# Kernel tuning notes

Measured on AMD Instinct MI355X. Metric: run time of the kernel, lower is better.

Reference implementation:

```python
import jax, jax.numpy as jnp
import numpy as np

EPS = 1e-5

def layer_norm(x, g, b):
    mu = jnp.mean(x, axis=-1, keepdims=True)
    var = jnp.mean((x - mu) ** 2, axis=-1, keepdims=True)
    return (x - mu) * jax.lax.rsqrt(var + EPS) * g + b

def setup_inputs() -> dict:
    key = jax.random.key(0)
    ks = jax.random.split(key, 12)
    P, D_IN, H, D_OUT, N = 2097152, 3, 64, 128, 65536
    x = jax.random.normal(ks[0], (P, D_IN), dtype=jnp.float32)
    batch_idx = jax.random.randint(ks[1], (P,), 0, N, dtype=jnp.int64)
    # mlp1: Linear(3,64) -> LN(64) -> ReLU -> Linear(64,64)
    W1 = jax.random.normal(ks[2], (D_IN, H), dtype=jnp.float32) * (1.0 / np.sqrt(D_IN))
    b1 = jnp.zeros((H,), jnp.float32)
    g1 = jnp.ones((H,), jnp.float32)
    be1 = jnp.zeros((H,), jnp.float32)
    W2 = jax.random.normal(ks[3], (H, H), dtype=jnp.float32) * (1.0 / np.sqrt(H))
    b2 = jnp.zeros((H,), jnp.float32)
    # mlp2: Linear(64,128) -> LN(128) -> ReLU -> Linear(128,128)
    W3 = jax.random.normal(ks[4], (H, D_OUT), dtype=jnp.float32) * (1.0 / np.sqrt(H))
    b3 = jnp.zeros((D_OUT,), jnp.float32)
    g2 = jnp.ones((D_OUT,), jnp.float32)
    be2 = jnp.zeros((D_OUT,), jnp.float32)
    W4 = jax.random.normal(ks[5], (D_OUT, D_OUT), dtype=jnp.float32) * (1.0 / np.sqrt(D_OUT))
    b4 = jnp.zeros((D_OUT,), jnp.float32)
    return {"x": x, "batch_idx": batch_idx, "num_nodes": N,
            "W1": W1, "b1": b1, "g1": g1, "be1": be1, "W2": W2, "b2": b2,
            "W3": W3, "b3": b3, "g2": g2, "be2": be2, "W4": W4, "b4": b4}

def reference(x, batch_idx, num_nodes, W1, b1, g1, be1, W2, b2, W3, b3, g2, be2, W4, b4):
    # per-point MLP1: [P,3] -> [P,64]
    h = jax.nn.relu(layer_norm(x @ W1 + b1, g1, be1)) @ W2 + b2
    # scatter_max pooling over unsorted batch_idx -> [num_nodes, 64]
    seg = jax.ops.segment_max(h, batch_idx, num_segments=num_nodes)
    counts = jax.ops.segment_sum(jnp.ones((h.shape[0],), h.dtype), batch_idx, num_segments=num_nodes)
    # torch_scatter.scatter_max leaves empty segments at 0
    seg = jnp.where(counts[:, None] > 0, seg, 0.0)
    # MLP2: [N,64] -> [N,128]
    out = jax.nn.relu(layer_norm(seg @ W3 + b3, g2, be2)) @ W4 + b4
    return out
```

## Files before the change

### kernel.cpp

```cpp
#include <hip/hip_runtime.h>
#include <hip/hip_bf16.h>
#include <math.h>

#define EPS_LN 1e-5f

typedef __attribute__((ext_vector_type(8))) short bf16x8;
typedef __attribute__((ext_vector_type(4))) float f32x4;
typedef __attribute__((ext_vector_type(2))) unsigned short u16x2;

__device__ __forceinline__ unsigned short f2bf(float f) {
    __hip_bfloat16 h = __float2bfloat16(f);
    return *reinterpret_cast<unsigned short*>(&h);
}
__device__ __forceinline__ float bf2f(unsigned short u) {
    return __uint_as_float(((unsigned)u) << 16);
}
__device__ __forceinline__ unsigned short ok16(float f) {
    unsigned short t = f2bf(f);
    unsigned short mask = (unsigned short)(((short)t) >> 15);
    return (unsigned short)(t ^ (unsigned short)(mask | 0x8000u));
}
__device__ __forceinline__ float decseg(unsigned o) {
    if (o == 0u) return 0.f;
    unsigned k = o >> 16;
    unsigned h = (k & 0x8000u) ? (k & 0x7FFFu) : (~k & 0xFFFFu);
    return bf2f((unsigned short)h);
}

__global__ __launch_bounds__(256) void prep_kernel(
    const float* __restrict__ W1, const float* __restrict__ b1,
    const float* __restrict__ g1, const float* __restrict__ be1,
    const float* __restrict__ W2,
    const float* __restrict__ W3, const float* __restrict__ W4,
    float* __restrict__ pW1e, float* __restrict__ pGB, float* __restrict__ pSG,
    unsigned short* __restrict__ pW2t,
    unsigned short* __restrict__ W3th, unsigned short* __restrict__ W3tl,
    unsigned short* __restrict__ W4th, unsigned short* __restrict__ W4tl)
{
    const int tid = threadIdx.x;
    if (tid < 64) {
        pW1e[4 * tid + 0] = W1[tid];
        pW1e[4 * tid + 1] = W1[64 + tid];
        pW1e[4 * tid + 2] = W1[128 + tid];
        pW1e[4 * tid + 3] = b1[tid];
        pGB[2 * tid + 0] = g1[tid];
        pGB[2 * tid + 1] = be1[tid];
    }
    if (tid >= 64 && tid < 78) {
        const int t = tid - 64;
        auto wcomp = [&](int k, int i) -> float {
            return (i < 3) ? W1[i * 64 + k] : b1[k];
        };
        if (t < 4) {
            float s = 0.f;
            for (int k = 0; k < 64; k++) s += wcomp(k, t);
            pSG[t] = s;
        } else {
            const int pi[10] = {0,0,0,0,1,1,1,2,2,3};
            const int pj[10] = {0,1,2,3,1,2,3,2,3,3};
            int p = t - 4;
            float s = 0.f;
            for (int k = 0; k < 64; k++) s += wcomp(k, pi[p]) * wcomp(k, pj[p]);
            pSG[4 + p] = s;
        }
    }
    for (int i = tid; i < 4096; i += 256) {
        int k = i >> 6, n = i & 63;
        pW2t[n * 72 + k] = f2bf(W2[i]);
    }
    for (int i = tid; i < 64 * 8; i += 256) {
        int n = i >> 3, k = 64 + (i & 7);
        pW2t[n * 72 + k] = 0;
    }
    for (int i = tid; i < 8192; i += 256) {
        int k = i >> 7, n = i & 127;
        float w = W3[k * 128 + n];
        unsigned short h = f2bf(w);
        W3th[n * 64 + k] = h;
        W3tl[n * 64 + k] = f2bf(w - bf2f(h));
    }
    for (int i = tid; i < 16384; i += 256) {
        int k = i >> 7, n = i & 127;
        float w = W4[k * 128 + n];
        unsigned short h = f2bf(w);
        W4th[n * 128 + k] = h;
        W4tl[n * 128 + k] = f2bf(w - bf2f(h));
    }
}

__global__ __launch_bounds__(256) void s1_count(const int* __restrict__ bidx,
                                                unsigned* __restrict__ blockHist, int P) {
    __shared__ unsigned hist[2048];
    const int tid = threadIdx.x;
    for (int i = tid; i < 2048; i += 256) hist[i] = 0;
    __syncthreads();
    const int base = blockIdx.x * 4096;
#pragma unroll
    for (int j = 0; j < 4; j++) {
        const int p0 = base + j * 1024 + tid * 4;
        if (p0 + 3 < P) {
            int4 n4 = *(const int4*)(bidx + p0);
            atomicAdd(&hist[((unsigned)n4.x) >> 5], 1u);
            atomicAdd(&hist[((unsigned)n4.y) >> 5], 1u);
            atomicAdd(&hist[((unsigned)n4.z) >> 5], 1u);
            atomicAdd(&hist[((unsigned)n4.w) >> 5], 1u);
        } else {
            for (int p = p0; p < P && p < p0 + 4; p++)
                atomicAdd(&hist[((unsigned)bidx[p]) >> 5], 1u);
        }
    }
    __syncthreads();
    unsigned* dst = blockHist + (size_t)blockIdx.x * 2048;
    for (int i = tid; i < 2048; i += 256) dst[i] = hist[i];
}

__global__ __launch_bounds__(256) void s2a_total(const unsigned* __restrict__ blockHist,
                                                 unsigned* __restrict__ binTotal, int nblk) {
    const int bin = blockIdx.x;
    const int tid = threadIdx.x;
    unsigned s = 0;
    for (int b = tid; b < nblk; b += 256) s += blockHist[(size_t)b * 2048 + bin];
    for (int off = 32; off; off >>= 1) s += __shfl_down(s, off);
    __shared__ unsigned ws[4];
    if ((tid & 63) == 0) ws[tid >> 6] = s;
    __syncthreads();
    if (tid == 0) binTotal[bin] = ws[0] + ws[1] + ws[2] + ws[3];
}

__global__ __launch_bounds__(1024) void s2b_scan(const unsigned* __restrict__ binTotal,
                                                 unsigned* __restrict__ partBase,
                                                 int nparts, int P) {
    __shared__ unsigned wtot[16];
    const int t = threadIdx.x;
    const unsigned c0 = (2 * t < nparts) ? binTotal[2 * t] : 0u;
    const unsigned c1 = (2 * t + 1 < nparts) ? binTotal[2 * t + 1] : 0u;
    const unsigned s = c0 + c1;
    unsigned v = s;
    const int lane = t & 63;
    for (int off = 1; off < 64; off <<= 1) {
        unsigned u = __shfl_up(v, off);
        if (lane >= off) v += u;
    }
    if (lane == 63) wtot[t >> 6] = v;
    __syncthreads();
    if (t == 0) {
        unsigned a = 0;
        for (int w = 0; w < 16; w++) { unsigned tmp = wtot[w]; wtot[w] = a; a += tmp; }
    }
    __syncthreads();
    const unsigned excl = wtot[t >> 6] + (v - s);
    if (2 * t < nparts) partBase[2 * t] = excl;
    if (2 * t + 1 < nparts) partBase[2 * t + 1] = excl + c0;
    if (t == 0) partBase[nparts] = (unsigned)P;
}

__global__ __launch_bounds__(256) void s2c_cursor(unsigned* __restrict__ blockHist,
                                                  const unsigned* __restrict__ partBase,
                                                  int nblk) {
    __shared__ unsigned wt0[4], wb0[4], wt1[4], wb1[4], tot0s;
    const int bin = blockIdx.x;
    const int tid = threadIdx.x;
    const int lane = tid & 63;
    const unsigned c0 = (tid < nblk) ? blockHist[(size_t)tid * 2048 + bin] : 0u;
    const unsigned c1 = (tid + 256 < nblk) ? blockHist[(size_t)(tid + 256) * 2048 + bin] : 0u;

    unsigned v0 = c0;
    for (int off = 1; off < 64; off <<= 1) {
        unsigned u = __shfl_up(v0, off);
        if (lane >= off) v0 += u;
    }
    if (lane == 63) wt0[tid >> 6] = v0;
    unsigned v1 = c1;
    for (int off = 1; off < 64; off <<= 1) {
        unsigned u = __shfl_up(v1, off);
        if (lane >= off) v1 += u;
    }
    if (lane == 63) wt1[tid >> 6] = v1;
    __syncthreads();
    if (tid == 0) {
        unsigned a = 0;
        for (int i = 0; i < 4; i++) { unsigned tmp = wt0[i]; wb0[i] = a; a += tmp; }
        tot0s = a;
        a = 0;
        for (int i = 0; i < 4; i++) { unsigned tmp = wt1[i]; wb1[i] = a; a += tmp; }
    }
    __syncthreads();
    const unsigned pb = partBase[bin];
    const unsigned e0 = pb + wb0[tid >> 6] + (v0 - c0);
    const unsigned e1 = pb + tot0s + wb1[tid >> 6] + (v1 - c1);
    if (tid < nblk) blockHist[(size_t)tid * 2048 + bin] = e0;
    if (tid + 256 < nblk) blockHist[(size_t)(tid + 256) * 2048 + bin] = e1;
}

__global__ __launch_bounds__(256) void s3_scatter(const int* __restrict__ bidx,
                                                  const float* __restrict__ x,
                                                  const unsigned* __restrict__ blockCursor,
                                                  float4* __restrict__ xb, int P) {
    __shared__ unsigned cur[2048];
    const int tid = threadIdx.x;
    const unsigned* src = blockCursor + (size_t)blockIdx.x * 2048;
    for (int i = tid; i < 2048; i += 256) cur[i] = src[i];
    __syncthreads();
    const int base = blockIdx.x * 4096;
#pragma unroll
    for (int j = 0; j < 4; j++) {
        const int p0 = base + j * 1024 + tid * 4;
        if (p0 + 3 < P) {
            int4 n4 = *(const int4*)(bidx + p0);
            const float4* xv = (const float4*)(x + 3 * (size_t)p0);
            float4 a = xv[0], b = xv[1], c = xv[2];
            const float xs[12] = {a.x, a.y, a.z, a.w, b.x, b.y, b.z, b.w,
                                  c.x, c.y, c.z, c.w};
            const unsigned nn[4] = {(unsigned)n4.x, (unsigned)n4.y,
                                    (unsigned)n4.z, (unsigned)n4.w};
#pragma unroll
            for (int u = 0; u < 4; u++) {
                const unsigned dst = atomicAdd(&cur[nn[u] >> 5], 1u);
                xb[dst] = make_float4(xs[3 * u], xs[3 * u + 1], xs[3 * u + 2],
                                      __uint_as_float(nn[u]));
            }
        } else {
            for (int u = 0; u < 4; u++) {
                const int p = p0 + u;
                if (p < P) {
                    const unsigned n = (unsigned)bidx[p];
                    const unsigned dst = atomicAdd(&cur[n >> 5], 1u);
                    xb[dst] = make_float4(x[3 * p], x[3 * p + 1], x[3 * p + 2],
                                          __uint_as_float(n));
                }
            }
        }
    }
}

__global__ __launch_bounds__(256) void s4_csr(const unsigned* __restrict__ partBase,
                                              unsigned* __restrict__ offsets,
                                              float4* __restrict__ xb, int N) {
    __shared__ float4 stage[1600];
    __shared__ unsigned hist[32], cur[32];
    const int tid = threadIdx.x;
    const int p = blockIdx.x;
    const unsigned start = partBase[p], end = partBase[p + 1];
    unsigned cnt = end - start;
    if (cnt > 1600u) cnt = 1600u;
    if (tid < 32) hist[tid] = 0;
    __syncthreads();
    for (unsigned k = tid; k < cnt; k += 256) {
        float4 r = xb[start + k];
        stage[k] = r;
        atomicAdd(&hist[__float_as_uint(r.w) & 31u], 1u);
    }
    __syncthreads();
    if (tid < 64) {
        const unsigned c = (tid < 32) ? hist[tid] : 0u;
        unsigned v = c;
        for (int off = 1; off < 32; off <<= 1) {
            unsigned u = __shfl_up(v, off);
            if (tid >= off) v += u;
        }
        if (tid < 32) {
            const unsigned excl = v - c;
            const int node = p * 32 + tid;
            if (node < N) offsets[node] = start + excl;
            cur[tid] = start + excl;
            if (node == N - 1) offsets[N] = start + excl + c;
        }
    }
    __syncthreads();
    for (unsigned k = tid; k < cnt; k += 256) {
        float4 r = stage[k];
        const unsigned dst = atomicAdd(&cur[__float_as_uint(r.w) & 31u], 1u);
        xb[dst] = r;
    }
}

__global__ __launch_bounds__(256, 2) void fused_mlp1_pool_kernel(
    const float4* __restrict__ xb, const unsigned* __restrict__ offsets,
    const float* __restrict__ pW1e, const float* __restrict__ pGB,
    const float* __restrict__ pSG, const unsigned short* __restrict__ pW2t,
    const float* __restrict__ b2,
    unsigned* __restrict__ segord, int P)
{
    __shared__ __align__(16) unsigned short sW2t[64 * 72];
    __shared__ __align__(16) unsigned short sa[256 * 72];
    __shared__ __align__(16) unsigned short shbt[64 * 260];
    __shared__ unsigned sn01[2];

    const int tid = threadIdx.x;
    {
        const uint4* src = (const uint4*)pW2t;
        uint4* dst = (uint4*)sW2t;
        for (int i = tid; i < 576; i += 256) dst[i] = src[i];
    }

    const int base = blockIdx.x * 256;
    const int row  = tid;
    const int pos  = base + row;
    const bool valid = (pos < P);

    float x0 = 0.f, x1 = 0.f, x2 = 0.f;
    if (valid) {
        float4 v = xb[pos];
        x0 = v.x; x1 = v.y; x2 = v.z;
        unsigned node = __float_as_uint(v.w);
        if (row == 0) sn01[0] = node;
        if (row == 255 || pos == P - 1) sn01[1] = node;
    }
    __syncthreads();

    {
        const float S0 = pSG[0], S1 = pSG[1], S2 = pSG[2], S3 = pSG[3];
        const float g00 = pSG[4], g01 = pSG[5], g02 = pSG[6], g03 = pSG[7];
        const float g11 = pSG[8], g12 = pSG[9], g13 = pSG[10];
        const float g22 = pSG[11], g23 = pSG[12], g33 = pSG[13];

        const float mu = fmaf(S0, x0, fmaf(S1, x1, fmaf(S2, x2, S3))) * (1.f / 64.f);
        float q = g33;
        q = fmaf(g00, x0 * x0, q);
        q = fmaf(g11, x1 * x1, q);
        q = fmaf(g22, x2 * x2, q);
        float c = fmaf(g01, x1, fmaf(g02, x2, g03));
        q = fmaf(2.f * x0, c, q);
        q = fmaf(2.f * x1, fmaf(g12, x2, g13), q);
        q = fmaf(2.f * x2, g23, q);
        float var = q * (1.f / 64.f) - mu * mu;
        var = var > 0.f ? var : 0.f;
        const float rs = rsqrtf(var + EPS_LN);
        const float r2 = -mu * rs;

        const float4* pw = (const float4*)pW1e;
        const float2* pg = (const float2*)pGB;
#pragma unroll
        for (int kb = 0; kb < 8; kb++) {
            bf16x8 v;
#pragma unroll
            for (int u = 0; u < 8; u++) {
                const int k = kb * 8 + u;
                float4 w = pw[k];
                float2 gb = pg[k];
                float y = fmaf(x0, w.x, fmaf(x1, w.y, fmaf(x2, w.z, w.w)));
                float tn = fmaf(y, rs, r2);
                float aa = fmaf(tn, gb.x, gb.y);
                aa = aa > 0.f ? aa : 0.f;
                v[u] = (short)f2bf(aa);
            }
            *reinterpret_cast<bf16x8*>(&sa[row * 72 + kb * 8]) = v;
        }
    }

    {
        const int wv   = tid >> 6;
        const int lane = tid & 63;
        const int m    = lane & 15;
        const int quad = lane >> 4;

        bf16x8 bfrag[4][2];
        float bc[4];
#pragma unroll
        for (int nt = 0; nt < 4; nt++) {
            bc[nt] = b2[nt * 16 + m];
#pragma unroll
            for (int s = 0; s < 2; s++)
                bfrag[nt][s] = *reinterpret_cast<const bf16x8*>(
                    &sW2t[(nt * 16 + m) * 72 + s * 32 + quad * 8]);
        }

#pragma unroll
        for (int rt = 0; rt < 4; rt++) {
            const int arow = wv * 64 + rt * 16 + m;
            bf16x8 af0 = *reinterpret_cast<const bf16x8*>(&sa[arow * 72 + quad * 8]);
            bf16x8 af1 = *reinterpret_cast<const bf16x8*>(&sa[arow * 72 + 32 + quad * 8]);
            const int orow = wv * 64 + rt * 16 + quad * 4;
#pragma unroll
            for (int nt = 0; nt < 4; nt++) {
                f32x4 acc = {bc[nt], bc[nt], bc[nt], bc[nt]};
                acc = __builtin_amdgcn_mfma_f32_16x16x32_bf16(af0, bfrag[nt][0], acc, 0, 0, 0);
                acc = __builtin_amdgcn_mfma_f32_16x16x32_bf16(af1, bfrag[nt][1], acc, 0, 0, 0);
                const int col = nt * 16 + m;
                uint2 pk;
                pk.x = (unsigned)ok16(acc[0]) | ((unsigned)ok16(acc[1]) << 16);
                pk.y = (unsigned)ok16(acc[2]) | ((unsigned)ok16(acc[3]) << 16);
                *reinterpret_cast<uint2*>(&shbt[col * 260 + orow]) = pk;
            }
        }
    }
    __syncthreads();

    const int nValid = (P - base < 256) ? (P - base) : 256;
    if (nValid <= 0) return;
    const unsigned n0 = sn01[0];
    const unsigned n1 = sn01[1];
    const unsigned bEnd = (unsigned)(base + nValid);
    const int wave = tid >> 6;
    const int ch   = tid & 63;
    const unsigned short* rowp = &shbt[ch * 260];

    for (unsigned n = n0 + (unsigned)wave; n <= n1; n += 4) {
        const unsigned s = offsets[n];
        const unsigned e = offsets[n + 1];
        int lo = (int)(s > (unsigned)base ? s : (unsigned)base) - base;
        int hi = (int)(e < bEnd ? e : bEnd) - base;
        if (hi <= lo) continue;
        u16x2 accv = {0, 0};
        unsigned short accs = 0;
        for (int r = lo & ~3; r < hi; r += 4) {
            uint2 d = *reinterpret_cast<const uint2*>(rowp + r);
            if (r >= lo && r + 4 <= hi) {
                u16x2 a = __builtin_bit_cast(u16x2, d.x);
                u16x2 b = __builtin_bit_cast(u16x2, d.y);
                accv = __builtin_elementwise_max(accv, __builtin_elementwise_max(a, b));
            } else {
                unsigned short v0 = (unsigned short)(d.x & 0xFFFFu);
                unsigned short v1 = (unsigned short)(d.x >> 16);
                unsigned short v2 = (unsigned short)(d.y & 0xFFFFu);
                unsigned short v3 = (unsigned short)(d.y >> 16);
                if (r     >= lo && r     < hi && v0 > accs) accs = v0;
                if (r + 1 >= lo && r + 1 < hi && v1 > accs) accs = v1;
                if (r + 2 >= lo && r + 2 < hi && v2 > accs) accs = v2;
                if (r + 3 >= lo && r + 3 < hi && v3 > accs) accs = v3;
            }
        }
        unsigned short k = accv.x > accv.y ? accv.x : accv.y;
        if (accs > k) k = accs;
        const unsigned key = ((unsigned)k) << 16;
        unsigned* dst = &segord[(size_t)n * 64 + ch];
        if (s >= (unsigned)base && e <= bEnd) *dst = key;
        else atomicMax(dst, key);
    }
}

__global__ __launch_bounds__(256) void mlp2_mfma_kernel(
    const unsigned* __restrict__ segord,
    const unsigned short* __restrict__ W3th, const unsigned short* __restrict__ W3tl,
    const unsigned short* __restrict__ W4th, const unsigned short* __restrict__ W4tl,
    const float* __restrict__ b3, const float* __restrict__ g2,
    const float* __restrict__ be2, const float* __restrict__ b4,
    float* __restrict__ out, int N)
{
    __shared__ __align__(16) unsigned short sa2[32 * 72];
    __shared__ __align__(16) float st[32 * 132];
    __shared__ __align__(16) unsigned short suh[32 * 136];
    __shared__ __align__(16) unsigned short sul[32 * 136];
    __shared__ float2 sred[32][8];
    __shared__ float sg2[128], sbe2[128];

    const int tid  = threadIdx.x;
    const int wv   = tid >> 6;
    const int lane = tid & 63;
    const int m    = lane & 15;
    const int quad = lane >> 4;

    if (tid < 128) { sg2[tid] = g2[tid]; sbe2[tid] = be2[tid]; }

    bf16x8 fw3h[2][2], fw3l[2][2];
    bf16x8 fw4h[2][4], fw4l[2][4];
    float bias3[2], bias4[2];
#pragma unroll
    for (int nti = 0; nti < 2; nti++) {
        const int nrow = (wv * 2 + nti) * 16 + m;
        bias3[nti] = b3[nrow];
        bias4[nti] = b4[nrow];
#pragma unroll
        for (int ks = 0; ks < 2; ks++) {
            fw3h[nti][ks] = *reinterpret_cast<const bf16x8*>(&W3th[nrow * 64 + ks * 32 + quad * 8]);
            fw3l[nti][ks] = *reinterpret_cast<const bf16x8*>(&W3tl[nrow * 64 + ks * 32 + quad * 8]);
        }
#pragma unroll
        for (int ks = 0; ks < 4; ks++) {
            fw4h[nti][ks] = *reinterpret_cast<const bf16x8*>(&W4th[nrow * 128 + ks * 32 + quad * 8]);
            fw4l[nti][ks] = *reinterpret_cast<const bf16x8*>(&W4tl[nrow * 128 + ks * 32 + quad * 8]);
        }
    }
    __syncthreads();

    for (int nb = blockIdx.x * 32; nb < N; nb += gridDim.x * 32) {
        {
            const int node = tid >> 3;
            const int k8   = (tid & 7) * 8;
            const uint4* sp = (const uint4*)&segord[(size_t)(nb + node) * 64 + k8];
            uint4 q0 = sp[0], q1 = sp[1];
            bf16x8 v;
            v[0] = (short)f2bf(decseg(q0.x));
            v[1] = (short)f2bf(decseg(q0.y));
            v[2] = (short)f2bf(decseg(q0.z));
            v[3] = (short)f2bf(decseg(q0.w));
            v[4] = (short)f2bf(decseg(q1.x));
            v[5] = (short)f2bf(decseg(q1.y));
            v[6] = (short)f2bf(decseg(q1.z));
            v[7] = (short)f2bf(decseg(q1.w));
            *reinterpret_cast<bf16x8*>(&sa2[node * 72 + k8]) = v;
        }
        __syncthreads();

#pragma unroll
        for (int mt = 0; mt < 2; mt++) {
            bf16x8 a0 = *reinterpret_cast<const bf16x8*>(&sa2[(mt * 16 + m) * 72 + quad * 8]);
            bf16x8 a1 = *reinterpret_cast<const bf16x8*>(&sa2[(mt * 16 + m) * 72 + 32 + quad * 8]);
#pragma unroll
            for (int nti = 0; nti < 2; nti++) {
                f32x4 acc = {bias3[nti], bias3[nti], bias3[nti], bias3[nti]};
                acc = __builtin_amdgcn_mfma_f32_16x16x32_bf16(a0, fw3h[nti][0], acc, 0, 0, 0);
                acc = __builtin_amdgcn_mfma_f32_16x16x32_bf16(a1, fw3h[nti][1], acc, 0, 0, 0);
                acc = __builtin_amdgcn_mfma_f32_16x16x32_bf16(a0, fw3l[nti][0], acc, 0, 0, 0);
                acc = __builtin_amdgcn_mfma_f32_16x16x32_bf16(a1, fw3l[nti][1], acc, 0, 0, 0);
#pragma unroll
                for (int r = 0; r < 4; r++)
                    st[(mt * 16 + quad * 4 + r) * 132 + (wv * 2 + nti) * 16 + m] = acc[r];
            }
        }
        __syncthreads();

        {
            const int node = tid >> 3;
            const int seg  = tid & 7;
            const float4* rp = (const float4*)&st[node * 132 + seg * 16];
            float4 v0 = rp[0], v1 = rp[1], v2 = rp[2], v3 = rp[3];
            float s1 = v0.x + v0.y + v0.z + v0.w + v1.x + v1.y + v1.z + v1.w
                     + v2.x + v2.y + v2.z + v2.w + v3.x + v3.y + v3.z + v3.w;
            float s2 = 0.f;
            s2 = fmaf(v0.x, v0.x, s2); s2 = fmaf(v0.y, v0.y, s2); s2 = fmaf(v0.z, v0.z, s2); s2 = fmaf(v0.w, v0.w, s2);
            s2 = fmaf(v1.x, v1.x, s2); s2 = fmaf(v1.y, v1.y, s2); s2 = fmaf(v1.z, v1.z, s2); s2 = fmaf(v1.w, v1.w, s2);
            s2 = fmaf(v2.x, v2.x, s2); s2 = fmaf(v2.y, v2.y, s2); s2 = fmaf(v2.z, v2.z, s2); s2 = fmaf(v2.w, v2.w, s2);
            s2 = fmaf(v3.x, v3.x, s2); s2 = fmaf(v3.y, v3.y, s2); s2 = fmaf(v3.z, v3.z, s2); s2 = fmaf(v3.w, v3.w, s2);
            sred[node][seg] = make_float2(s1, s2);
            __syncthreads();

            float t1 = 0.f, t2 = 0.f;
#pragma unroll
            for (int i = 0; i < 8; i++) { float2 r = sred[node][i]; t1 += r.x; t2 += r.y; }
            const float mu  = t1 * (1.f / 128.f);
            float var = t2 * (1.f / 128.f) - mu * mu;
            var = var > 0.f ? var : 0.f;
            const float rsd = rsqrtf(var + EPS_LN);

            float tv[16] = {v0.x, v0.y, v0.z, v0.w, v1.x, v1.y, v1.z, v1.w,
                            v2.x, v2.y, v2.z, v2.w, v3.x, v3.y, v3.z, v3.w};
            bf16x8 vh[2], vl[2];
#pragma unroll
            for (int i = 0; i < 16; i++) {
                const int j = seg * 16 + i;
                float u = fmaf((tv[i] - mu) * rsd, sg2[j], sbe2[j]);
                u = u > 0.f ? u : 0.f;
                unsigned short uh = f2bf(u);
                unsigned short ul = f2bf(u - bf2f(uh));
                vh[i >> 3][i & 7] = (short)uh;
                vl[i >> 3][i & 7] = (short)ul;
            }
            *reinterpret_cast<bf16x8*>(&suh[node * 136 + seg * 16])     = vh[0];
            *reinterpret_cast<bf16x8*>(&suh[node * 136 + seg * 16 + 8]) = vh[1];
            *reinterpret_cast<bf16x8*>(&sul[node * 136 + seg * 16])     = vl[0];
            *reinterpret_cast<bf16x8*>(&sul[node * 136 + seg * 16 + 8]) = vl[1];
        }
        __syncthreads();

#pragma unroll
        for (int mt = 0; mt < 2; mt++) {
            bf16x8 ah[4], al[4];
#pragma unroll
            for (int ks = 0; ks < 4; ks++) {
                ah[ks] = *reinterpret_cast<const bf16x8*>(&suh[(mt * 16 + m) * 136 + ks * 32 + quad * 8]);
                al[ks] = *reinterpret_cast<const bf16x8*>(&sul[(mt * 16 + m) * 136 + ks * 32 + quad * 8]);
            }
#pragma unroll
            for (int nti = 0; nti < 2; nti++) {
                f32x4 acc = {bias4[nti], bias4[nti], bias4[nti], bias4[nti]};
#pragma unroll
                for (int ks = 0; ks < 4; ks++) {
                    acc = __builtin_amdgcn_mfma_f32_16x16x32_bf16(ah[ks], fw4h[nti][ks], acc, 0, 0, 0);
                    acc = __builtin_amdgcn_mfma_f32_16x16x32_bf16(al[ks], fw4h[nti][ks], acc, 0, 0, 0);
                    acc = __builtin_amdgcn_mfma_f32_16x16x32_bf16(ah[ks], fw4l[nti][ks], acc, 0, 0, 0);
                }
#pragma unroll
                for (int r = 0; r < 4; r++) {
                    const int node = nb + mt * 16 + quad * 4 + r;
                    if (node < N)
                        out[(size_t)node * 128 + (wv * 2 + nti) * 16 + m] = acc[r];
                }
            }
        }
        __syncthreads();
    }
}

extern "C" void kernel_launch(void* const* d_in, const int* in_sizes, int n_in,
                              void* d_out, int out_size, void* d_ws, size_t ws_size,
                              hipStream_t stream) {
    const float* x    = (const float*)d_in[0];
    const int*   bidx = (const int*)d_in[1];
    const float* W1  = (const float*)d_in[3];
    const float* b1  = (const float*)d_in[4];
    const float* g1  = (const float*)d_in[5];
    const float* be1 = (const float*)d_in[6];
    const float* W2  = (const float*)d_in[7];
    const float* b2  = (const float*)d_in[8];
    const float* W3  = (const float*)d_in[9];
    const float* b3  = (const float*)d_in[10];
    const float* g2  = (const float*)d_in[11];
    const float* be2 = (const float*)d_in[12];
    const float* W4  = (const float*)d_in[13];
    const float* b4  = (const float*)d_in[14];

    const int P = in_sizes[0] / 3;
    const int N = out_size / 128;
    const int nparts = (N + 31) >> 5;
    const int nblk   = (P + 4095) / 4096;

    uintptr_t w = (uintptr_t)d_ws;
    auto align = [](uintptr_t v) { return (v + 255) & ~(uintptr_t)255; };
    unsigned* blockHist = (unsigned*)align(w);     w = (uintptr_t)(blockHist + (size_t)nblk * 2048);
    unsigned* binTotal  = (unsigned*)align(w);     w = (uintptr_t)(binTotal  + 2048);
    unsigned* partBase  = (unsigned*)align(w);     w = (uintptr_t)(partBase  + 2049);
    unsigned* offsets   = (unsigned*)align(w);     w = (uintptr_t)(offsets   + N + 1);
    float4*   xb        = (float4*)align(w);       w = (uintptr_t)(xb        + P);
    unsigned* segord    = (unsigned*)align(w);     w = (uintptr_t)(segord    + (size_t)N * 64);
    float*    pW1e      = (float*)align(w);        w = (uintptr_t)(pW1e      + 256);
    float*    pGB       = (float*)align(w);        w = (uintptr_t)(pGB       + 128);
    float*    pSG       = (float*)align(w);        w = (uintptr_t)(pSG       + 16);
    unsigned short* pW2t = (unsigned short*)align(w); w = (uintptr_t)(pW2t + 64 * 72);
    unsigned short* W3th = (unsigned short*)align(w); w = (uintptr_t)(W3th + 128 * 64);
    unsigned short* W3tl = (unsigned short*)align(w); w = (uintptr_t)(W3tl + 128 * 64);
    unsigned short* W4th = (unsigned short*)align(w); w = (uintptr_t)(W4th + 128 * 128);
    unsigned short* W4tl = (unsigned short*)align(w); w = (uintptr_t)(W4tl + 128 * 128);

    hipMemsetAsync(segord, 0, (size_t)N * 64 * sizeof(unsigned), stream);

    prep_kernel<<<1, 256, 0, stream>>>(W1, b1, g1, be1, W2, W3, W4,
                                       pW1e, pGB, pSG, pW2t, W3th, W3tl, W4th, W4tl);

    s1_count<<<nblk, 256, 0, stream>>>(bidx, blockHist, P);
    s2a_total<<<nparts, 256, 0, stream>>>(blockHist, binTotal, nblk);
    s2b_scan<<<1, 1024, 0, stream>>>(binTotal, partBase, nparts, P);
    s2c_cursor<<<nparts, 256, 0, stream>>>(blockHist, partBase, nblk);
    s3_scatter<<<nblk, 256, 0, stream>>>(bidx, x, blockHist, xb, P);
    s4_csr<<<nparts, 256, 0, stream>>>(partBase, offsets, xb, N);

    fused_mlp1_pool_kernel<<<(P + 255) / 256, 256, 0, stream>>>(
        xb, offsets, pW1e, pGB, pSG, pW2t, b2, segord, P);

    mlp2_mfma_kernel<<<512, 256, 0, stream>>>(
        segord, W3th, W3tl, W4th, W4tl, b3, g2, be2, b4, (float*)d_out, N);
}
```

Before: 372.0 us.

## Build MFMA A-fragments in registers via shuffles, drop W2/activation LDS staging

Computes the MLP1 first-layer activations directly into MFMA A-operand register layout, using lane shuffles to broadcast each row's inputs and LN stats, and loads the W2 B-fragments straight from global memory. This removes the sW2t and sa shared-memory buffers, one barrier, and the LDS round trip. LDS use drops, so launch bounds are raised to 4 blocks per CU for occupancy. In exchange, each lane recomputes layer-1 values for four rows, which adds shuffles and ALU work and raises register pressure.

```diff
diff --git a/kernel.cpp b/kernel.cpp
--- a/kernel.cpp
+++ b/kernel.cpp
@@ -7,6 +7,7 @@
 typedef __attribute__((ext_vector_type(8))) short bf16x8;
 typedef __attribute__((ext_vector_type(4))) float f32x4;
 typedef __attribute__((ext_vector_type(2))) unsigned short u16x2;
+typedef __attribute__((ext_vector_type(4))) unsigned int u32x4;
 
 __device__ __forceinline__ unsigned short f2bf(float f) {
     __hip_bfloat16 h = __float2bfloat16(f);
@@ -274,40 +275,46 @@
     }
 }
 
-__global__ __launch_bounds__(256, 2) void fused_mlp1_pool_kernel(
+__global__ __launch_bounds__(256, 4) void fused_mlp1_pool_kernel(
     const float4* __restrict__ xb, const unsigned* __restrict__ offsets,
     const float* __restrict__ pW1e, const float* __restrict__ pGB,
     const float* __restrict__ pSG, const unsigned short* __restrict__ pW2t,
     const float* __restrict__ b2,
     unsigned* __restrict__ segord, int P)
 {
-    __shared__ __align__(16) unsigned short sW2t[64 * 72];
-    __shared__ __align__(16) unsigned short sa[256 * 72];
     __shared__ __align__(16) unsigned short shbt[64 * 260];
     __shared__ unsigned sn01[2];
 
-    const int tid = threadIdx.x;
-    {
-        const uint4* src = (const uint4*)pW2t;
-        uint4* dst = (uint4*)sW2t;
-        for (int i = tid; i < 576; i += 256) dst[i] = src[i];
-    }
-
+    const int tid  = threadIdx.x;
+    const int wv   = tid >> 6;
+    const int lane = tid & 63;
+    const int m    = lane & 15;
+    const int quad = lane >> 4;
     const int base = blockIdx.x * 256;
-    const int row  = tid;
-    const int pos  = base + row;
+    const int pos  = base + tid;
     const bool valid = (pos < P);
+
+    bf16x8 bfrag[4][2];
+    float bc[4];
+#pragma unroll
+    for (int nt = 0; nt < 4; nt++) {
+        bc[nt] = b2[nt * 16 + m];
+#pragma unroll
+        for (int s = 0; s < 2; s++)
+            bfrag[nt][s] = *reinterpret_cast<const bf16x8*>(
+                &pW2t[(nt * 16 + m) * 72 + s * 32 + quad * 8]);
+    }
 
     float x0 = 0.f, x1 = 0.f, x2 = 0.f;
     if (valid) {
         float4 v = xb[pos];
         x0 = v.x; x1 = v.y; x2 = v.z;
         unsigned node = __float_as_uint(v.w);
-        if (row == 0) sn01[0] = node;
-        if (row == 255 || pos == P - 1) sn01[1] = node;
-    }
-    __syncthreads();
-
+        if (tid == 0) sn01[0] = node;
+        if (tid == 255 || pos == P - 1) sn01[1] = node;
+    }
+
+    float rs, r2;
     {
         const float S0 = pSG[0], S1 = pSG[1], S2 = pSG[2], S3 = pSG[3];
         const float g00 = pSG[4], g01 = pSG[5], g02 = pSG[6], g03 = pSG[7];
@@ -325,63 +332,63 @@
         q = fmaf(2.f * x2, g23, q);
         float var = q * (1.f / 64.f) - mu * mu;
         var = var > 0.f ? var : 0.f;
-        const float rs = rsqrtf(var + EPS_LN);
-        const float r2 = -mu * rs;
-
+        rs = rsqrtf(var + EPS_LN);
+        r2 = -mu * rs;
+    }
+
+    float xr0[4], xr1[4], xr2[4], rsr[4], r2r[4];
+#pragma unroll
+    for (int rt = 0; rt < 4; rt++) {
+        const int src = rt * 16 + m;
+        xr0[rt] = __shfl(x0, src);
+        xr1[rt] = __shfl(x1, src);
+        xr2[rt] = __shfl(x2, src);
+        rsr[rt] = __shfl(rs, src);
+        r2r[rt] = __shfl(r2, src);
+    }
+
+    u32x4 afr[4][2];
+    {
         const float4* pw = (const float4*)pW1e;
         const float2* pg = (const float2*)pGB;
 #pragma unroll
-        for (int kb = 0; kb < 8; kb++) {
-            bf16x8 v;
-#pragma unroll
-            for (int u = 0; u < 8; u++) {
-                const int k = kb * 8 + u;
-                float4 w = pw[k];
-                float2 gb = pg[k];
-                float y = fmaf(x0, w.x, fmaf(x1, w.y, fmaf(x2, w.z, w.w)));
-                float tn = fmaf(y, rs, r2);
-                float aa = fmaf(tn, gb.x, gb.y);
-                aa = aa > 0.f ? aa : 0.f;
-                v[u] = (short)f2bf(aa);
-            }
-            *reinterpret_cast<bf16x8*>(&sa[row * 72 + kb * 8]) = v;
-        }
-    }
-
-    {
-        const int wv   = tid >> 6;
-        const int lane = tid & 63;
-        const int m    = lane & 15;
-        const int quad = lane >> 4;
-
-        bf16x8 bfrag[4][2];
-        float bc[4];
+        for (int s = 0; s < 2; s++) {
+#pragma unroll
+            for (int up = 0; up < 4; up++) {
+                const int ch = s * 32 + quad * 8 + up * 2;
+                const float4 wA = pw[ch], wB = pw[ch + 1];
+                const float2 gA = pg[ch], gB = pg[ch + 1];
+#pragma unroll
+                for (int rt = 0; rt < 4; rt++) {
+                    float y0 = fmaf(xr0[rt], wA.x, fmaf(xr1[rt], wA.y,
+                               fmaf(xr2[rt], wA.z, wA.w)));
+                    float y1 = fmaf(xr0[rt], wB.x, fmaf(xr1[rt], wB.y,
+                               fmaf(xr2[rt], wB.z, wB.w)));
+                    float a0 = fmaf(fmaf(y0, rsr[rt], r2r[rt]), gA.x, gA.y);
+                    float a1 = fmaf(fmaf(y1, rsr[rt], r2r[rt]), gB.x, gB.y);
+                    a0 = a0 > 0.f ? a0 : 0.f;
+                    a1 = a1 > 0.f ? a1 : 0.f;
+                    afr[rt][s][up] = (unsigned)f2bf(a0) | ((unsigned)f2bf(a1) << 16);
+                }
+            }
+        }
+    }
+
+#pragma unroll
+    for (int rt = 0; rt < 4; rt++) {
+        const int orow = wv * 64 + rt * 16 + quad * 4;
+        const bf16x8 af0 = __builtin_bit_cast(bf16x8, afr[rt][0]);
+        const bf16x8 af1 = __builtin_bit_cast(bf16x8, afr[rt][1]);
 #pragma unroll
         for (int nt = 0; nt < 4; nt++) {
-            bc[nt] = b2[nt * 16 + m];
-#pragma unroll
-            for (int s = 0; s < 2; s++)
-                bfrag[nt][s] = *reinterpret_cast<const bf16x8*>(
-                    &sW2t[(nt * 16 + m) * 72 + s * 32 + quad * 8]);
-        }
-
-#pragma unroll
-        for (int rt = 0; rt < 4; rt++) {
-            const int arow = wv * 64 + rt * 16 + m;
-            bf16x8 af0 = *reinterpret_cast<const bf16x8*>(&sa[arow * 72 + quad * 8]);
-            bf16x8 af1 = *reinterpret_cast<const bf16x8*>(&sa[arow * 72 + 32 + quad * 8]);
-            const int orow = wv * 64 + rt * 16 + quad * 4;
-#pragma unroll
-            for (int nt = 0; nt < 4; nt++) {
-                f32x4 acc = {bc[nt], bc[nt], bc[nt], bc[nt]};
-                acc = __builtin_amdgcn_mfma_f32_16x16x32_bf16(af0, bfrag[nt][0], acc, 0, 0, 0);
-                acc = __builtin_amdgcn_mfma_f32_16x16x32_bf16(af1, bfrag[nt][1], acc, 0, 0, 0);
-                const int col = nt * 16 + m;
-                uint2 pk;
-                pk.x = (unsigned)ok16(acc[0]) | ((unsigned)ok16(acc[1]) << 16);
-                pk.y = (unsigned)ok16(acc[2]) | ((unsigned)ok16(acc[3]) << 16);
-                *reinterpret_cast<uint2*>(&shbt[col * 260 + orow]) = pk;
-            }
+            f32x4 acc = {bc[nt], bc[nt], bc[nt], bc[nt]};
+            acc = __builtin_amdgcn_mfma_f32_16x16x32_bf16(af0, bfrag[nt][0], acc, 0, 0, 0);
+            acc = __builtin_amdgcn_mfma_f32_16x16x32_bf16(af1, bfrag[nt][1], acc, 0, 0, 0);
+            const int col = nt * 16 + m;
+            uint2 pk;
+            pk.x = (unsigned)ok16(acc[0]) | ((unsigned)ok16(acc[1]) << 16);
+            pk.y = (unsigned)ok16(acc[2]) | ((unsigned)ok16(acc[3]) << 16);
+            *reinterpret_cast<uint2*>(&shbt[col * 260 + orow]) = pk;
         }
     }
     __syncthreads();
```

New measurement: 340.3 us. 1.09x faster.
